# Kernel optimization log

Hardware: AMD Instinct MI355X
Metric: run time of the kernel (lower is better)

The kernel has to match this reference:

```python
import jax, jax.numpy as jnp
import numpy as np

SEQ, D_IN, D_OUT = 8192, 1024, 1024

def setup_inputs() -> dict:
    key = jax.random.key(0)
    kx, kq, kk, kv = jax.random.split(key, 4)
    x = jax.random.normal(kx, (SEQ, D_IN), dtype=jnp.float32)
    # original uses torch.rand (uniform [0,1)) for parameters
    W_query = jax.random.uniform(kq, (D_IN, D_OUT), dtype=jnp.float32)
    W_key = jax.random.uniform(kk, (D_IN, D_OUT), dtype=jnp.float32)
    W_value = jax.random.uniform(kv, (D_IN, D_OUT), dtype=jnp.float32)
    return {"x": x, "W_query": W_query, "W_key": W_key, "W_value": W_value}

def reference(x, W_query, W_key, W_value):
    # x: [S, d_in]; projections: [S, d_out]
    queries = x @ W_query
    keys = x @ W_key
    values = x @ W_value
    scale = 1.0 / jnp.sqrt(jnp.asarray(keys.shape[-1], dtype=x.dtype))
    attn_scores = jnp.einsum('sd,td->st', queries, keys) * scale  # [S, S]
    attn_weights = jax.nn.softmax(attn_scores, axis=-1)
    context_vec = attn_weights @ values  # [S, d_out]
    return context_vec
```

## Files before the change

### kernel.cpp

```cpp
#include <hip/hip_runtime.h>
#include <hip/hip_bf16.h>
#include <hip/hip_fp16.h>

#define SEQ 8192
#define DM  1024

typedef __attribute__((ext_vector_type(8))) short    bf16x8;
typedef __attribute__((ext_vector_type(8))) _Float16 f16x8;
typedef __attribute__((ext_vector_type(4))) float    f32x4;

union H8 { _Float16 h[8]; int4 v; };

__device__ __forceinline__ unsigned short f2bf(float f) {
    union { float f; unsigned u; } x; x.f = f;
    unsigned r = x.u + 0x7fffu + ((x.u >> 16) & 1u);
    return (unsigned short)(r >> 16);
}
__device__ __forceinline__ float bf2f(unsigned short h) {
    union { unsigned u; float f; } x; x.u = ((unsigned)h) << 16;
    return x.f;
}

__device__ __forceinline__ void gld16(const unsigned short* g, unsigned short* l) {
    __builtin_amdgcn_global_load_lds(
        (const __attribute__((address_space(1))) void*)g,
        (__attribute__((address_space(3))) void*)l, 16, 0, 0);
}

__global__ __launch_bounds__(256) void prep_kernel(const float* __restrict__ x,
    unsigned short* __restrict__ xhi, unsigned short* __restrict__ xlo,
    const float* W0, const float* W1, const float* W2,
    unsigned short* H0, unsigned short* L0,
    unsigned short* H1, unsigned short* L1,
    unsigned short* H2, unsigned short* L2)
{
    __shared__ float tile[64][65];
    int t = threadIdx.x;

    if (blockIdx.x < 8192) {
        int base = (blockIdx.x * 256 + t) * 4;
        float4 v = *(const float4*)(x + base);
        float f[4] = {v.x, v.y, v.z, v.w};
        unsigned short h[4], l[4];
#pragma unroll
        for (int j = 0; j < 4; j++) { h[j] = f2bf(f[j]); l[j] = f2bf(f[j] - bf2f(h[j])); }
        ushort4 hv = {h[0], h[1], h[2], h[3]};
        ushort4 lv = {l[0], l[1], l[2], l[3]};
        *(ushort4*)(xhi + base) = hv;
        *(ushort4*)(xlo + base) = lv;
        return;
    }

    int id = blockIdx.x - 8192;
    int z  = id >> 8;
    int rem = id & 255;
    int bn = (rem & 15) * 64;
    int bk = (rem >> 4) * 64;
    const float* W = (z == 0) ? W0 : (z == 1) ? W1 : W2;
    unsigned short* Wthi = (z == 0) ? H0 : (z == 1) ? H1 : H2;
    unsigned short* Wtlo = (z == 0) ? L0 : (z == 1) ? L1 : L2;

#pragma unroll
    for (int p = 0; p < 4; p++) {
        int r = p * 16 + (t >> 4);
        int c = (t & 15) * 4;
        float4 v = *(const float4*)(W + (size_t)(bk + r) * DM + bn + c);
        tile[r][c] = v.x; tile[r][c+1] = v.y; tile[r][c+2] = v.z; tile[r][c+3] = v.w;
    }
    __syncthreads();
#pragma unroll
    for (int p = 0; p < 2; p++) {
        int task = p * 256 + t;
        int rn = task >> 3;
        int kc = (task & 7) * 8;
        union { unsigned short u[8]; int4 v; } hh, ll;
#pragma unroll
        for (int j = 0; j < 8; j++) {
            float f = tile[kc + j][rn];
            hh.u[j] = f2bf(f);
            ll.u[j] = f2bf(f - bf2f(hh.u[j]));
        }
        size_t o = (size_t)(bn + rn) * DM + bk + kc;
        *(int4*)(Wthi + o) = hh.v;
        *(int4*)(Wtlo + o) = ll.v;
    }
}

template<int MODE, int KD>
__global__ __launch_bounds__(256, 2) void gemm128(
    const unsigned short* A,   const unsigned short* Alo,
    const unsigned short* B_,  const unsigned short* Blo_,
    const unsigned short* B2,  const unsigned short* B2lo,
    unsigned short* Chi_, unsigned short* Clo_,
    unsigned short* Chi2, unsigned short* Clo2,
    _Float16* Cf16, float* Cf32, const float* __restrict__ Scp)
{
    constexpr bool SPLIT = (MODE == 0);
    constexpr int NT = KD / 32;
    __shared__ alignas(16) unsigned short sAhi[2][128 * 32];
    __shared__ alignas(16) unsigned short sBhi[2][128 * 32];
    __shared__ alignas(16) unsigned short sAlo[SPLIT ? 2 * 128 * 32 : 16];
    __shared__ alignas(16) unsigned short sBlo[SPLIT ? 2 * 128 * 32 : 16];
    __shared__ alignas(16) _Float16 sSc[(MODE == 3) ? 128 * 130 : 8];

    const unsigned short* B   = B_;
    const unsigned short* Blo = Blo_;
    unsigned short* Chi = Chi_;
    unsigned short* Clo = Clo_;
    if (MODE == 0 && blockIdx.z == 1) { B = B2; Blo = B2lo; Chi = Chi2; Clo = Clo2; }

    const int m0 = blockIdx.x * 128;
    const int n0 = blockIdx.y * 128;
    const int t = threadIdx.x;
    const int wave = t >> 6, lane = t & 63;
    const int wr = wave >> 1, wc = wave & 1;
    const int i16 = lane & 15, quad = lane >> 4;

    const int rs = wave * 32 + (lane >> 2);
    const int scol = ((lane & 3) ^ ((lane >> 3) & 3)) << 3;
    const size_t aoff = (size_t)(m0 + rs) * KD + scol;
    const size_t boff = (size_t)(n0 + rs) * KD + scol;
    const int ldsb = wave * 1024;

    int offA[4], offB[4];
#pragma unroll
    for (int mt = 0; mt < 4; mt++) {
        int row = wr * 64 + mt * 16 + i16;
        offA[mt] = row * 32 + ((quad ^ ((row >> 1) & 3)) << 3);
    }
#pragma unroll
    for (int nt = 0; nt < 4; nt++) {
        int row = wc * 64 + nt * 16 + i16;
        offB[nt] = row * 32 + ((quad ^ ((row >> 1) & 3)) << 3);
    }

    if constexpr (MODE == 3) {
#pragma unroll
        for (int i = 0; i < 16; i++) {
            int idx = i * 1024 + t * 4;
            int row = idx >> 7, col = idx & 127;
            float4 v = *(const float4*)(Scp + (size_t)(m0 + row) * 128 + col);
            _Float16* d = sSc + row * 130 + col;
            d[0] = (_Float16)v.x; d[1] = (_Float16)v.y;
            d[2] = (_Float16)v.z; d[3] = (_Float16)v.w;
        }
    }

    auto STAGE = [&](int buf, int k) {
        gld16(A + aoff + k,           sAhi[buf] + ldsb);
        gld16(A + aoff + 16 * KD + k, sAhi[buf] + ldsb + 512);
        gld16(B + boff + k,           sBhi[buf] + ldsb);
        gld16(B + boff + 16 * KD + k, sBhi[buf] + ldsb + 512);
        if constexpr (SPLIT) {
            gld16(Alo + aoff + k,           sAlo + buf * 4096 + ldsb);
            gld16(Alo + aoff + 16 * KD + k, sAlo + buf * 4096 + ldsb + 512);
            gld16(Blo + boff + k,           sBlo + buf * 4096 + ldsb);
            gld16(Blo + boff + 16 * KD + k, sBlo + buf * 4096 + ldsb + 512);
        }
    };

    f32x4 acc[4][4] = {};

    STAGE(0, 0);
    __syncthreads();

    for (int kt = 0; kt < NT; ++kt) {
        const int cur = kt & 1;
        const int k = kt * 32;

        bf16x8 ahi[4], alo[4], bhi[4], blo[4];
#pragma unroll
        for (int mt = 0; mt < 4; mt++) {
            ahi[mt] = *(const bf16x8*)(sAhi[cur] + offA[mt]);
            if constexpr (SPLIT) alo[mt] = *(const bf16x8*)(sAlo + cur * 4096 + offA[mt]);
        }
#pragma unroll
        for (int nt = 0; nt < 4; nt++) {
            bhi[nt] = *(const bf16x8*)(sBhi[cur] + offB[nt]);
            if constexpr (SPLIT) blo[nt] = *(const bf16x8*)(sBlo + cur * 4096 + offB[nt]);
        }
        if constexpr (MODE == 3) {
#pragma unroll
            for (int mt = 0; mt < 4; mt++) {
                _Float16 sc = sSc[(wr * 64 + mt * 16 + i16) * 130 + (k >> 6)];
                f16x8 av = __builtin_bit_cast(f16x8, ahi[mt]);
                av = av * sc;
                ahi[mt] = __builtin_bit_cast(bf16x8, av);
            }
        }

        if (kt + 1 < NT) STAGE(cur ^ 1, k + 32);

        __builtin_amdgcn_s_setprio(1);
#pragma unroll
        for (int nt = 0; nt < 4; nt++)
#pragma unroll
            for (int mt = 0; mt < 4; mt++) {
                if constexpr (MODE == 3) {
                    acc[mt][nt] = __builtin_amdgcn_mfma_f32_16x16x32_f16(
                        __builtin_bit_cast(f16x8, ahi[mt]), __builtin_bit_cast(f16x8, bhi[nt]),
                        acc[mt][nt], 0, 0, 0);
                } else {
                    acc[mt][nt] = __builtin_amdgcn_mfma_f32_16x16x32_bf16(ahi[mt], bhi[nt], acc[mt][nt], 0, 0, 0);
                    if constexpr (SPLIT) {
                        acc[mt][nt] = __builtin_amdgcn_mfma_f32_16x16x32_bf16(ahi[mt], blo[nt], acc[mt][nt], 0, 0, 0);
                        acc[mt][nt] = __builtin_amdgcn_mfma_f32_16x16x32_bf16(alo[mt], bhi[nt], acc[mt][nt], 0, 0, 0);
                    }
                }
            }
        __builtin_amdgcn_s_setprio(0);

        asm volatile("s_waitcnt vmcnt(0)" ::: "memory");
        __builtin_amdgcn_s_barrier();
        __builtin_amdgcn_sched_barrier(0);
    }

    if constexpr (MODE == 0) {
#pragma unroll
        for (int mt = 0; mt < 4; mt++)
#pragma unroll
            for (int nt = 0; nt < 4; nt++)
#pragma unroll
                for (int r = 0; r < 4; r++) {
                    int row = m0 + wr * 64 + mt * 16 + quad * 4 + r;
                    int col = n0 + wc * 64 + nt * 16 + i16;
                    float v = acc[mt][nt][r];
                    unsigned short h = f2bf(v);
                    Chi[(size_t)row * DM + col] = h;
                    Clo[(size_t)row * DM + col] = f2bf(v - bf2f(h));
                }
    } else if constexpr (MODE == 1) {
#pragma unroll
        for (int mt = 0; mt < 4; mt++)
#pragma unroll
            for (int nt = 0; nt < 4; nt++) {
                int row0 = m0 + wr * 64 + mt * 16 + quad * 4;
                int col  = n0 + wc * 64 + nt * 16 + i16;
                union { _Float16 h[4]; ushort2 u2[2]; unsigned long long q; } p;
#pragma unroll
                for (int r = 0; r < 4; r++) p.h[r] = (_Float16)acc[mt][nt][r];
                *(unsigned long long*)(Cf16 + (size_t)col * SEQ + row0) = p.q;
            }
    } else {
#pragma unroll
        for (int mt = 0; mt < 4; mt++)
#pragma unroll
            for (int nt = 0; nt < 4; nt++)
#pragma unroll
                for (int r = 0; r < 4; r++) {
                    int row = m0 + wr * 64 + mt * 16 + quad * 4 + r;
                    int col = n0 + wc * 64 + nt * 16 + i16;
                    Cf32[(size_t)row * DM + col] = acc[mt][nt][r];
                }
    }
}

__global__ __launch_bounds__(512, 2) void scores256(
    const unsigned short* __restrict__ Qh, const unsigned short* __restrict__ Ql,
    const unsigned short* __restrict__ Kh, const unsigned short* __restrict__ Kl,
    _Float16* __restrict__ Eo, float* __restrict__ Tt, float* __restrict__ Zt)
{
    constexpr int KD = 1024;
    constexpr int NT = KD / 32;
    __shared__ alignas(16) unsigned short lds[2 * 4 * 8192];

    const int flat = blockIdx.y * gridDim.x + blockIdx.x;
    const int wg = (flat & 7) * 128 + (flat >> 3);
    const int m0 = (wg >> 5) << 8;
    const int n0 = (wg & 31) << 8;

    const int t = threadIdx.x;
    const int wave = t >> 6, lane = t & 63;
    const int wr = wave >> 2, wc = wave & 3;
    const int i16 = lane & 15, quad = lane >> 4;

    const int srow = wave * 16 + (lane >> 2);
    const int scol = ((lane & 3) ^ ((lane >> 3) & 3)) << 3;
    const size_t ga = (size_t)(m0 + srow) * KD + scol;
    const size_t gb = (size_t)(n0 + srow) * KD + scol;
    const int ldw = wave * 512;

    int offA[8], offB[4];
#pragma unroll
    for (int mt = 0; mt < 8; mt++) {
        int row = wr * 128 + mt * 16 + i16;
        offA[mt] = row * 32 + ((quad ^ ((row >> 1) & 3)) << 3);
    }
#pragma unroll
    for (int nt = 0; nt < 4; nt++) {
        int row = wc * 64 + nt * 16 + i16;
        offB[nt] = row * 32 + ((quad ^ ((row >> 1) & 3)) << 3);
    }

    f32x4 acc[8][4] = {};

    auto STAGE = [&](int buf, int kt) {
        unsigned short* p = lds + buf * 32768;
        const int k = kt * 32;
#pragma unroll
        for (int i = 0; i < 2; i++) {
            const size_t gAo = ga + (size_t)(i * 128) * KD + k;
            const size_t gBo = gb + (size_t)(i * 128) * KD + k;
            const int lo = ldw + i * 4096;
            gld16(Qh + gAo, p + lo);
            gld16(Ql + gAo, p + 8192  + lo);
            gld16(Kh + gBo, p + 16384 + lo);
            gld16(Kl + gBo, p + 24576 + lo);
        }
    };

    STAGE(0, 0);
    asm volatile("s_waitcnt vmcnt(0)" ::: "memory");
    __builtin_amdgcn_s_barrier();
    __builtin_amdgcn_sched_barrier(0);

    for (int kt = 0; kt < NT; ++kt) {
        const int cur = kt & 1;
        const unsigned short* pAh = lds + cur * 32768;
        const unsigned short* pAl = pAh + 8192;
        const unsigned short* pBh = pAh + 16384;
        const unsigned short* pBl = pAh + 24576;

        bf16x8 ah[4], al[4], bh[4], bl[4];

#pragma unroll
        for (int mi = 0; mi < 4; mi++) {
            ah[mi] = *(const bf16x8*)(pAh + offA[mi]);
            al[mi] = *(const bf16x8*)(pAl + offA[mi]);
        }
#pragma unroll
        for (int ni = 0; ni < 4; ni++) {
            bh[ni] = *(const bf16x8*)(pBh + offB[ni]);
            bl[ni] = *(const bf16x8*)(pBl + offB[ni]);
        }
        if (kt + 1 < NT) STAGE(cur ^ 1, kt + 1);

        __builtin_amdgcn_s_setprio(1);
#pragma unroll
        for (int mi = 0; mi < 4; mi++)
#pragma unroll
            for (int ni = 0; ni < 4; ni++) {
                f32x4 c = acc[mi][ni];
                c = __builtin_amdgcn_mfma_f32_16x16x32_bf16(ah[mi], bh[ni], c, 0, 0, 0);
                c = __builtin_amdgcn_mfma_f32_16x16x32_bf16(ah[mi], bl[ni], c, 0, 0, 0);
                c = __builtin_amdgcn_mfma_f32_16x16x32_bf16(al[mi], bh[ni], c, 0, 0, 0);
                acc[mi][ni] = c;
            }
        __builtin_amdgcn_s_setprio(0);

#pragma unroll
        for (int mi = 0; mi < 4; mi++) {
            ah[mi] = *(const bf16x8*)(pAh + offA[4 + mi]);
            al[mi] = *(const bf16x8*)(pAl + offA[4 + mi]);
        }

        __builtin_amdgcn_s_setprio(1);
#pragma unroll
        for (int mi = 0; mi < 4; mi++)
#pragma unroll
            for (int ni = 0; ni < 4; ni++) {
                f32x4 c = acc[4 + mi][ni];
                c = __builtin_amdgcn_mfma_f32_16x16x32_bf16(ah[mi], bh[ni], c, 0, 0, 0);
                c = __builtin_amdgcn_mfma_f32_16x16x32_bf16(ah[mi], bl[ni], c, 0, 0, 0);
                c = __builtin_amdgcn_mfma_f32_16x16x32_bf16(al[mi], bh[ni], c, 0, 0, 0);
                acc[4 + mi][ni] = c;
            }
        __builtin_amdgcn_s_setprio(0);

        asm volatile("s_waitcnt vmcnt(0)" ::: "memory");
        __builtin_amdgcn_s_barrier();
        __builtin_amdgcn_sched_barrier(0);
    }

    const float scale = 0.03125f;
    const int tix = (n0 + wc * 64) >> 6;
#pragma unroll
    for (int mt = 0; mt < 8; mt++)
#pragma unroll
        for (int r = 0; r < 4; r++) {
            float s0 = acc[mt][0][r] * scale, s1 = acc[mt][1][r] * scale;
            float s2 = acc[mt][2][r] * scale, s3 = acc[mt][3][r] * scale;
            float mx = fmaxf(fmaxf(s0, s1), fmaxf(s2, s3));
            mx = fmaxf(mx, __shfl_xor(mx, 1));
            mx = fmaxf(mx, __shfl_xor(mx, 2));
            mx = fmaxf(mx, __shfl_xor(mx, 4));
            mx = fmaxf(mx, __shfl_xor(mx, 8));
            float e0 = __expf(s0 - mx), e1 = __expf(s1 - mx);
            float e2 = __expf(s2 - mx), e3 = __expf(s3 - mx);
            float z = e0 + e1 + e2 + e3;
            z += __shfl_xor(z, 1);
            z += __shfl_xor(z, 2);
            z += __shfl_xor(z, 4);
            z += __shfl_xor(z, 8);
            int row = m0 + wr * 128 + mt * 16 + quad * 4 + r;
            if (i16 == 0) {
                Tt[(size_t)row * 128 + tix] = mx;
                Zt[(size_t)row * 128 + tix] = z;
            }
            size_t eb = (size_t)row * SEQ + n0 + wc * 64 + i16;
            Eo[eb +  0] = (_Float16)e0;
            Eo[eb + 16] = (_Float16)e1;
            Eo[eb + 32] = (_Float16)e2;
            Eo[eb + 48] = (_Float16)e3;
        }
}

__global__ __launch_bounds__(256) void sc_reduce(const float* __restrict__ Tt,
    const float* __restrict__ Zt, float* __restrict__ Sc)
{
    int row = blockIdx.x * 4 + (threadIdx.x >> 6);
    int lane = threadIdx.x & 63;
    size_t b = (size_t)row * 128 + lane;
    float t0 = Tt[b], t1 = Tt[b + 64];
    float z0 = Zt[b], z1 = Zt[b + 64];
    float m = fmaxf(t0, t1);
    for (int sh = 1; sh < 64; sh <<= 1) m = fmaxf(m, __shfl_xor(m, sh));
    float l = z0 * __expf(t0 - m) + z1 * __expf(t1 - m);
    for (int sh = 1; sh < 64; sh <<= 1) l += __shfl_xor(l, sh);
    float inv = 1.0f / l;
    Sc[b]      = __expf(t0 - m) * inv;
    Sc[b + 64] = __expf(t1 - m) * inv;
}

extern "C" void kernel_launch(void* const* d_in, const int* in_sizes, int n_in,
                              void* d_out, int out_size, void* d_ws, size_t ws_size,
                              hipStream_t stream)
{
    const float* x  = (const float*)d_in[0];
    const float* Wq = (const float*)d_in[1];
    const float* Wk = (const float*)d_in[2];
    const float* Wv = (const float*)d_in[3];
    float* Out = (float*)d_out;
    char* ws = (char*)d_ws;

    const size_t MB = 1024 * 1024;
    unsigned short* xhi   = (unsigned short*)(ws + 0 * MB);
    unsigned short* xlo   = (unsigned short*)(ws + 16 * MB);
    unsigned short* Wqthi = (unsigned short*)(ws + 32 * MB);
    unsigned short* Wqtlo = (unsigned short*)(ws + 34 * MB);
    unsigned short* Wkthi = (unsigned short*)(ws + 36 * MB);
    unsigned short* Wktlo = (unsigned short*)(ws + 38 * MB);
    unsigned short* Wvthi = (unsigned short*)(ws + 40 * MB);
    unsigned short* Wvtlo = (unsigned short*)(ws + 42 * MB);
    _Float16*       E     = (_Float16*)     (ws + 0 * MB);

    size_t off = 128 * MB;
    unsigned short* Qhi = (unsigned short*)(ws + off); off += 16 * MB;
    unsigned short* Qlo = (unsigned short*)(ws + off); off += 16 * MB;
    unsigned short* Khi = (unsigned short*)(ws + off); off += 16 * MB;
    unsigned short* Klo = (unsigned short*)(ws + off); off += 16 * MB;
    _Float16*       Vt  = (_Float16*)      (ws + off); off += 16 * MB;
    float*          Tt  = (float*)         (ws + off); off += (size_t)SEQ * 128 * 4;
    float*          Zt  = (float*)         (ws + off); off += (size_t)SEQ * 128 * 4;
    float*          Sc  = (float*)         (ws + off); off += (size_t)SEQ * 128 * 4;

    prep_kernel<<<8192 + 768, 256, 0, stream>>>(x, xhi, xlo, Wq, Wk, Wv,
        Wqthi, Wqtlo, Wkthi, Wktlo, Wvthi, Wvtlo);
    gemm128<0, DM><<<dim3(SEQ / 128, DM / 128, 2), 256, 0, stream>>>(
        xhi, xlo, Wqthi, Wqtlo, Wkthi, Wktlo,
        Qhi, Qlo, Khi, Klo, nullptr, nullptr, nullptr);
    gemm128<1, DM><<<dim3(SEQ / 128, DM / 128), 256, 0, stream>>>(
        xhi, nullptr, Wvthi, nullptr, nullptr, nullptr,
        nullptr, nullptr, nullptr, nullptr, (_Float16*)Vt, nullptr, nullptr);
    scores256<<<dim3(SEQ / 256, SEQ / 256), 512, 0, stream>>>(
        Qhi, Qlo, Khi, Klo, E, Tt, Zt);
    sc_reduce<<<SEQ / 4, 256, 0, stream>>>(Tt, Zt, Sc);
    gemm128<3, SEQ><<<dim3(SEQ / 128, DM / 128), 256, 0, stream>>>(
        (const unsigned short*)E, nullptr, (const unsigned short*)Vt, nullptr, nullptr, nullptr,
        nullptr, nullptr, nullptr, nullptr, nullptr, Out, Sc);
}
```

Before: 692.1 us.

## Fold Wq·Wk^T into one small matrix and score against x directly

Builds G = Wq·Wk^T (a 1024x1024 product, stored minus a constant 256 offset in split bf16 hi/lo) and computes Y = x·G. Scores then become Y·x^T, plus a rank-one correction from per-row sums of x that restores the subtracted offset. This removes one of the two full-sequence projection GEMMs (Q and K) and replaces it with a tiny GEMM plus a row-sum reduction in the prep kernel. The cost is extra epilogue arithmetic and some accuracy risk from the reassociated products and the offset cancellation.

```diff
diff --git a/kernel.cpp b/kernel.cpp
--- a/kernel.cpp
+++ b/kernel.cpp
@@ -29,16 +29,18 @@
 
 __global__ __launch_bounds__(256) void prep_kernel(const float* __restrict__ x,
     unsigned short* __restrict__ xhi, unsigned short* __restrict__ xlo,
+    float* __restrict__ rsum,
     const float* W0, const float* W1, const float* W2,
-    unsigned short* H0, unsigned short* L0,
-    unsigned short* H1, unsigned short* L1,
+    unsigned short* Wqh, unsigned short* Wql,
+    unsigned short* Wkh, unsigned short* Wkl,
     unsigned short* H2, unsigned short* L2)
 {
     __shared__ float tile[64][65];
+    __shared__ float rbuf[4];
     int t = threadIdx.x;
 
     if (blockIdx.x < 8192) {
-        int base = (blockIdx.x * 256 + t) * 4;
+        int base = blockIdx.x * 1024 + t * 4;
         float4 v = *(const float4*)(x + base);
         float f[4] = {v.x, v.y, v.z, v.w};
         unsigned short h[4], l[4];
@@ -48,17 +50,37 @@
         ushort4 lv = {l[0], l[1], l[2], l[3]};
         *(ushort4*)(xhi + base) = hv;
         *(ushort4*)(xlo + base) = lv;
+        float s4 = f[0] + f[1] + f[2] + f[3];
+#pragma unroll
+        for (int sh = 1; sh < 64; sh <<= 1) s4 += __shfl_xor(s4, sh);
+        if ((t & 63) == 0) rbuf[t >> 6] = s4;
+        __syncthreads();
+        if (t == 0) rsum[blockIdx.x] = rbuf[0] + rbuf[1] + rbuf[2] + rbuf[3];
         return;
     }
 
-    int id = blockIdx.x - 8192;
-    int z  = id >> 8;
-    int rem = id & 255;
-    int bn = (rem & 15) * 64;
-    int bk = (rem >> 4) * 64;
-    const float* W = (z == 0) ? W0 : (z == 1) ? W1 : W2;
-    unsigned short* Wthi = (z == 0) ? H0 : (z == 1) ? H1 : H2;
-    unsigned short* Wtlo = (z == 0) ? L0 : (z == 1) ? L1 : L2;
+    if (blockIdx.x < 8192 + 2048) {
+        int id = blockIdx.x - 8192;
+        const float* W = (id < 1024) ? W0 : W1;
+        unsigned short* H = (id < 1024) ? Wqh : Wkh;
+        unsigned short* L = (id < 1024) ? Wql : Wkl;
+        int base = (id & 1023) * 1024 + t * 4;
+        float4 v = *(const float4*)(W + base);
+        float f[4] = {v.x, v.y, v.z, v.w};
+        unsigned short h[4], l[4];
+#pragma unroll
+        for (int j = 0; j < 4; j++) { h[j] = f2bf(f[j]); l[j] = f2bf(f[j] - bf2f(h[j])); }
+        ushort4 hv = {h[0], h[1], h[2], h[3]};
+        ushort4 lv = {l[0], l[1], l[2], l[3]};
+        *(ushort4*)(H + base) = hv;
+        *(ushort4*)(L + base) = lv;
+        return;
+    }
+
+    int id2 = blockIdx.x - 10240;
+    int bn = (id2 & 15) * 64;
+    int bk = (id2 >> 4) * 64;
+    const float* W = W2;
 
 #pragma unroll
     for (int p = 0; p < 4; p++) {
@@ -81,8 +103,8 @@
             ll.u[j] = f2bf(f - bf2f(hh.u[j]));
         }
         size_t o = (size_t)(bn + rn) * DM + bk + kc;
-        *(int4*)(Wthi + o) = hh.v;
-        *(int4*)(Wtlo + o) = ll.v;
+        *(int4*)(H2 + o) = hh.v;
+        *(int4*)(L2 + o) = ll.v;
     }
 }
 
@@ -90,12 +112,10 @@
 __global__ __launch_bounds__(256, 2) void gemm128(
     const unsigned short* A,   const unsigned short* Alo,
     const unsigned short* B_,  const unsigned short* Blo_,
-    const unsigned short* B2,  const unsigned short* B2lo,
-    unsigned short* Chi_, unsigned short* Clo_,
-    unsigned short* Chi2, unsigned short* Clo2,
+    unsigned short* Chi, unsigned short* Clo,
     _Float16* Cf16, float* Cf32, const float* __restrict__ Scp)
 {
-    constexpr bool SPLIT = (MODE == 0);
+    constexpr bool SPLIT = (MODE == 0 || MODE == 4);
     constexpr int NT = KD / 32;
     __shared__ alignas(16) unsigned short sAhi[2][128 * 32];
     __shared__ alignas(16) unsigned short sBhi[2][128 * 32];
@@ -105,9 +125,6 @@
 
     const unsigned short* B   = B_;
     const unsigned short* Blo = Blo_;
-    unsigned short* Chi = Chi_;
-    unsigned short* Clo = Clo_;
-    if (MODE == 0 && blockIdx.z == 1) { B = B2; Blo = B2lo; Chi = Chi2; Clo = Clo2; }
 
     const int m0 = blockIdx.x * 128;
     const int n0 = blockIdx.y * 128;
@@ -236,10 +253,28 @@
             for (int nt = 0; nt < 4; nt++) {
                 int row0 = m0 + wr * 64 + mt * 16 + quad * 4;
                 int col  = n0 + wc * 64 + nt * 16 + i16;
-                union { _Float16 h[4]; ushort2 u2[2]; unsigned long long q; } p;
+                union { _Float16 h[4]; unsigned long long q; } p;
 #pragma unroll
                 for (int r = 0; r < 4; r++) p.h[r] = (_Float16)acc[mt][nt][r];
                 *(unsigned long long*)(Cf16 + (size_t)col * SEQ + row0) = p.q;
+            }
+    } else if constexpr (MODE == 4) {
+#pragma unroll
+        for (int mt = 0; mt < 4; mt++)
+#pragma unroll
+            for (int nt = 0; nt < 4; nt++) {
+                int row0 = m0 + wr * 64 + mt * 16 + quad * 4;
+                int col  = n0 + wc * 64 + nt * 16 + i16;
+                union { unsigned short u[4]; unsigned long long q; } ph, pl;
+#pragma unroll
+                for (int r = 0; r < 4; r++) {
+                    float v = acc[mt][nt][r] - 256.0f;
+                    unsigned short h = f2bf(v);
+                    ph.u[r] = h;
+                    pl.u[r] = f2bf(v - bf2f(h));
+                }
+                *(unsigned long long*)(Chi + (size_t)col * DM + row0) = ph.q;
+                *(unsigned long long*)(Clo + (size_t)col * DM + row0) = pl.q;
             }
     } else {
 #pragma unroll
@@ -256,13 +291,15 @@
 }
 
 __global__ __launch_bounds__(512, 2) void scores256(
-    const unsigned short* __restrict__ Qh, const unsigned short* __restrict__ Ql,
-    const unsigned short* __restrict__ Kh, const unsigned short* __restrict__ Kl,
+    const unsigned short* __restrict__ Yh, const unsigned short* __restrict__ Yl,
+    const unsigned short* __restrict__ Xh, const unsigned short* __restrict__ Xl,
+    const float* __restrict__ rsum,
     _Float16* __restrict__ Eo, float* __restrict__ Tt, float* __restrict__ Zt)
 {
     constexpr int KD = 1024;
     constexpr int NT = KD / 32;
     __shared__ alignas(16) unsigned short lds[2 * 4 * 8192];
+    __shared__ float srM[256], srN[256];
 
     const int flat = blockIdx.y * gridDim.x + blockIdx.x;
     const int wg = (flat & 7) * 128 + (flat >> 3);
@@ -273,6 +310,9 @@
     const int wave = t >> 6, lane = t & 63;
     const int wr = wave >> 2, wc = wave & 3;
     const int i16 = lane & 15, quad = lane >> 4;
+
+    if (t < 256) srM[t] = rsum[m0 + t];
+    else         srN[t - 256] = rsum[n0 + t - 256];
 
     const int srow = wave * 16 + (lane >> 2);
     const int scol = ((lane & 3) ^ ((lane >> 3) & 3)) << 3;
@@ -302,10 +342,10 @@
             const size_t gAo = ga + (size_t)(i * 128) * KD + k;
             const size_t gBo = gb + (size_t)(i * 128) * KD + k;
             const int lo = ldw + i * 4096;
-            gld16(Qh + gAo, p + lo);
-            gld16(Ql + gAo, p + 8192  + lo);
-            gld16(Kh + gBo, p + 16384 + lo);
-            gld16(Kl + gBo, p + 24576 + lo);
+            gld16(Yh + gAo, p + lo);
+            gld16(Yl + gAo, p + 8192  + lo);
+            gld16(Xh + gBo, p + 16384 + lo);
+            gld16(Xl + gBo, p + 24576 + lo);
         }
     };
 
@@ -373,13 +413,21 @@
     }
 
     const float scale = 0.03125f;
+    const float RC = 8.0f;
     const int tix = (n0 + wc * 64) >> 6;
+    const float rn0 = RC * srN[wc * 64 + i16];
+    const float rn1 = RC * srN[wc * 64 + 16 + i16];
+    const float rn2 = RC * srN[wc * 64 + 32 + i16];
+    const float rn3 = RC * srN[wc * 64 + 48 + i16];
 #pragma unroll
     for (int mt = 0; mt < 8; mt++)
 #pragma unroll
         for (int r = 0; r < 4; r++) {
-            float s0 = acc[mt][0][r] * scale, s1 = acc[mt][1][r] * scale;
-            float s2 = acc[mt][2][r] * scale, s3 = acc[mt][3][r] * scale;
+            float rm = srM[wr * 128 + mt * 16 + quad * 4 + r];
+            float s0 = acc[mt][0][r] * scale + rm * rn0;
+            float s1 = acc[mt][1][r] * scale + rm * rn1;
+            float s2 = acc[mt][2][r] * scale + rm * rn2;
+            float s3 = acc[mt][3][r] * scale + rm * rn3;
             float mx = fmaxf(fmaxf(s0, s1), fmaxf(s2, s3));
             mx = fmaxf(mx, __shfl_xor(mx, 1));
             mx = fmaxf(mx, __shfl_xor(mx, 2));
@@ -434,38 +482,39 @@
     char* ws = (char*)d_ws;
 
     const size_t MB = 1024 * 1024;
-    unsigned short* xhi   = (unsigned short*)(ws + 0 * MB);
-    unsigned short* xlo   = (unsigned short*)(ws + 16 * MB);
-    unsigned short* Wqthi = (unsigned short*)(ws + 32 * MB);
-    unsigned short* Wqtlo = (unsigned short*)(ws + 34 * MB);
-    unsigned short* Wkthi = (unsigned short*)(ws + 36 * MB);
-    unsigned short* Wktlo = (unsigned short*)(ws + 38 * MB);
-    unsigned short* Wvthi = (unsigned short*)(ws + 40 * MB);
-    unsigned short* Wvtlo = (unsigned short*)(ws + 42 * MB);
-    _Float16*       E     = (_Float16*)     (ws + 0 * MB);
+    unsigned short* Wqh  = (unsigned short*)(ws + 0 * MB);
+    unsigned short* Wql  = (unsigned short*)(ws + 2 * MB);
+    unsigned short* Wkh  = (unsigned short*)(ws + 4 * MB);
+    unsigned short* Wkl  = (unsigned short*)(ws + 6 * MB);
+    unsigned short* Wvth = (unsigned short*)(ws + 8 * MB);
+    unsigned short* Wvtl = (unsigned short*)(ws + 10 * MB);
+    unsigned short* Ghi  = (unsigned short*)(ws + 12 * MB);
+    unsigned short* Glo  = (unsigned short*)(ws + 14 * MB);
+    _Float16*       E    = (_Float16*)     (ws + 0 * MB);
 
     size_t off = 128 * MB;
-    unsigned short* Qhi = (unsigned short*)(ws + off); off += 16 * MB;
-    unsigned short* Qlo = (unsigned short*)(ws + off); off += 16 * MB;
-    unsigned short* Khi = (unsigned short*)(ws + off); off += 16 * MB;
-    unsigned short* Klo = (unsigned short*)(ws + off); off += 16 * MB;
+    unsigned short* Yhi = (unsigned short*)(ws + off); off += 16 * MB;
+    unsigned short* Ylo = (unsigned short*)(ws + off); off += 16 * MB;
+    unsigned short* xhi = (unsigned short*)(ws + off); off += 16 * MB;
+    unsigned short* xlo = (unsigned short*)(ws + off); off += 16 * MB;
     _Float16*       Vt  = (_Float16*)      (ws + off); off += 16 * MB;
     float*          Tt  = (float*)         (ws + off); off += (size_t)SEQ * 128 * 4;
     float*          Zt  = (float*)         (ws + off); off += (size_t)SEQ * 128 * 4;
     float*          Sc  = (float*)         (ws + off); off += (size_t)SEQ * 128 * 4;
-
-    prep_kernel<<<8192 + 768, 256, 0, stream>>>(x, xhi, xlo, Wq, Wk, Wv,
-        Wqthi, Wqtlo, Wkthi, Wktlo, Wvthi, Wvtlo);
-    gemm128<0, DM><<<dim3(SEQ / 128, DM / 128, 2), 256, 0, stream>>>(
-        xhi, xlo, Wqthi, Wqtlo, Wkthi, Wktlo,
-        Qhi, Qlo, Khi, Klo, nullptr, nullptr, nullptr);
+    float*          rs  = (float*)         (ws + off); off += (size_t)SEQ * 4;
+
+    prep_kernel<<<8192 + 2048 + 256, 256, 0, stream>>>(x, xhi, xlo, rs, Wq, Wk, Wv,
+        Wqh, Wql, Wkh, Wkl, Wvth, Wvtl);
+    gemm128<4, DM><<<dim3(8, 8), 256, 0, stream>>>(
+        Wqh, Wql, Wkh, Wkl, Ghi, Glo, nullptr, nullptr, nullptr);
     gemm128<1, DM><<<dim3(SEQ / 128, DM / 128), 256, 0, stream>>>(
-        xhi, nullptr, Wvthi, nullptr, nullptr, nullptr,
-        nullptr, nullptr, nullptr, nullptr, (_Float16*)Vt, nullptr, nullptr);
+        xhi, nullptr, Wvth, nullptr, nullptr, nullptr, (_Float16*)Vt, nullptr, nullptr);
+    gemm128<0, DM><<<dim3(SEQ / 128, DM / 128), 256, 0, stream>>>(
+        xhi, xlo, Ghi, Glo, Yhi, Ylo, nullptr, nullptr, nullptr);
     scores256<<<dim3(SEQ / 256, SEQ / 256), 512, 0, stream>>>(
-        Qhi, Qlo, Khi, Klo, E, Tt, Zt);
+        Yhi, Ylo, xhi, xlo, rs, E, Tt, Zt);
     sc_reduce<<<SEQ / 4, 256, 0, stream>>>(Tt, Zt, Sc);
     gemm128<3, SEQ><<<dim3(SEQ / 128, DM / 128), 256, 0, stream>>>(
-        (const unsigned short*)E, nullptr, (const unsigned short*)Vt, nullptr, nullptr, nullptr,
-        nullptr, nullptr, nullptr, nullptr, nullptr, Out, Sc);
-}
+        (const unsigned short*)E, nullptr, (const unsigned short*)Vt, nullptr,
+        nullptr, nullptr, nullptr, Out, Sc);
+}
```

Result: slower. 706.2 us (+2.0%).
